# Kernel tuning notes

Hardware: AMD Instinct MI355X
Metric: run time of the kernel (lower is better)

Reference implementation:

```python
import jax, jax.numpy as jnp
import numpy as np


def fps(x, k):
    """Farthest point sampling. x: [B, N, D]. Returns int32 indices [B, k].
    Deterministic: first selected point is index 0 (torch repo uses randint init;
    we fix 0 for a reproducible baseline)."""
    B, N, D = x.shape
    binds = jnp.arange(B)

    def step(carry, _):
        dist, far = carry                      # dist: [B, N], far: [B]
        centroid = x[binds, far]               # [B, D]
        d = jnp.sum((x - centroid[:, None, :]) ** 2, axis=-1)  # [B, N]
        dist = jnp.minimum(dist, d)
        nxt = jnp.argmax(dist, axis=-1)
        return (dist, nxt), far

    init = (jnp.full((B, N), jnp.inf, dtype=x.dtype),
            jnp.zeros((B,), dtype=jnp.int32))
    _, idxs = jax.lax.scan(step, init, None, length=k)
    return idxs.T                              # [B, k]


def sine_mlp(x, params, w0=1.0):
    """Stack of 1x1 convs (== per-point linear) with sin(w0*.) activations.
    x: [B, N, C_in] -> [B, N, C_out]."""
    h = x
    for W, b in params:                        # W: [C_out, C_in], b: [C_out]
        h = jnp.sin(w0 * (jnp.einsum('bnc,oc->bno', h, W) + b))
    return h


_DIMS = [(6, 32), (32, 64), (64, 64), (64, 128), (128, 256), (256, 512)]


def setup_inputs() -> dict:
    key = jax.random.key(0)
    keys = jax.random.split(key, 1 + 2 * len(_DIMS))
    inp = {"x": jax.random.normal(keys[0], (16, 8192, 6), dtype=jnp.float32)}
    for i, (cin, cout) in enumerate(_DIMS):
        scale = 1.0 / np.sqrt(cin)
        inp[f"W{i+1}"] = jax.random.normal(keys[1 + 2 * i], (cout, cin), dtype=jnp.float32) * scale
        inp[f"b{i+1}"] = jax.random.normal(keys[2 + 2 * i], (cout,), dtype=jnp.float32) * 0.01
    inp["k"] = 1024
    return inp


def reference(x, W1, b1, W2, b2, W3, b3, W4, b4, W5, b5, W6, b6, k):
    params = [(W1, b1), (W2, b2), (W3, b3), (W4, b4), (W5, b5), (W6, b6)]
    sample_idx = fps(x, k)                     # [B, k] int32
    feat = sine_mlp(x, params)                 # [B, N, 512]
    # index_points gather along point dim, then permute back -> [B, k, 512]
    out = jnp.take_along_axis(feat, sample_idx[:, :, None], axis=1)
    return out
```

## Files before the change

### kernel.cpp

```cpp
#include <hip/hip_runtime.h>
#include <hip/hip_bf16.h>

#define NPTS 8192
#define KS   1024
#define NB   16
#define MLPB 2048

template<int NT, int JP, int CINP, int CINT, int COUT, int CT, bool LAST>
__device__ __forceinline__ void run_layer(const float* __restrict__ W,
                                          const float* __restrict__ bias,
                                          const float* __restrict__ in,
                                          float* __restrict__ outlds,
                                          float* __restrict__ gout,
                                          float* __restrict__ wt,
                                          int qbase, int tid) {
  constexpr int S = (COUT + 63) / 64;
  const int lane = tid & 63;
  const int wave = tid >> 6;
  const int p0   = wave * JP;

  float acc[JP][S];
  {
    float bv[S];
    #pragma unroll
    for (int s = 0; s < S; ++s) {
      int o = s * 64 + lane;
      bv[s] = (o < COUT) ? bias[o] : 0.f;
    }
    #pragma unroll
    for (int j = 0; j < JP; ++j)
      #pragma unroll
      for (int s = 0; s < S; ++s) acc[j][s] = bv[s];
  }

  for (int ct0 = 0; ct0 < CINT; ct0 += CT) {
    __syncthreads();
    #pragma unroll 1
    for (int e = tid; e < COUT * CT; e += NT) {
      int o  = e / CT;
      int cc = e % CT;
      wt[cc * (COUT + 1) + o] = W[o * CINT + ct0 + cc];
    }
    __syncthreads();
    #pragma unroll
    for (int cc0 = 0; cc0 < CT; cc0 += 4) {
      if (CT - cc0 >= 4) {
        float a[JP][4];
        #pragma unroll
        for (int j = 0; j < JP; ++j) {
          float4 t = *reinterpret_cast<const float4*>(&in[(p0 + j) * CINP + ct0 + cc0]);
          a[j][0] = t.x; a[j][1] = t.y; a[j][2] = t.z; a[j][3] = t.w;
        }
        #pragma unroll
        for (int u = 0; u < 4; ++u) {
          float wvv[S];
          #pragma unroll
          for (int s = 0; s < S; ++s)
            wvv[s] = wt[(cc0 + u) * (COUT + 1) + s * 64 + lane];
          #pragma unroll
          for (int j = 0; j < JP; ++j)
            #pragma unroll
            for (int s = 0; s < S; ++s)
              acc[j][s] = fmaf(a[j][u], wvv[s], acc[j][s]);
        }
      } else {
        float a[JP][2];
        #pragma unroll
        for (int j = 0; j < JP; ++j) {
          float2 t = *reinterpret_cast<const float2*>(&in[(p0 + j) * CINP + ct0 + cc0]);
          a[j][0] = t.x; a[j][1] = t.y;
        }
        #pragma unroll
        for (int u = 0; u < 2; ++u) {
          float wvv[S];
          #pragma unroll
          for (int s = 0; s < S; ++s)
            wvv[s] = wt[(cc0 + u) * (COUT + 1) + s * 64 + lane];
          #pragma unroll
          for (int j = 0; j < JP; ++j)
            #pragma unroll
            for (int s = 0; s < S; ++s)
              acc[j][s] = fmaf(a[j][u], wvv[s], acc[j][s]);
        }
      }
    }
  }
  #pragma unroll
  for (int j = 0; j < JP; ++j) {
    #pragma unroll
    for (int s = 0; s < S; ++s) {
      int o = s * 64 + lane;
      if (o < COUT) {
        float r = sinf(acc[j][s]);
        if (LAST) gout[(size_t)(qbase + p0 + j) * 512 + o] = r;
        else      outlds[(p0 + j) * COUT + o] = r;
      }
    }
  }
}

__device__ __forceinline__ void fps_body(const float* __restrict__ x,
                                         int* __restrict__ idx_out,
                                         unsigned long long* __restrict__ wvi,
                                         int b, int tid) {
#pragma clang fp contract(off)
  const int lane = tid & 63;
  const int wave = tid >> 6;
  const float* xb = x + (size_t)b * NPTS * 6;

  float crd[48];
  {
    const float4* src = reinterpret_cast<const float4*>(xb + tid * 48);
    #pragma unroll
    for (int i = 0; i < 12; ++i) {
      float4 v = src[i];
      crd[4*i+0] = v.x; crd[4*i+1] = v.y; crd[4*i+2] = v.z; crd[4*i+3] = v.w;
    }
  }
  #pragma unroll
  for (int i = 0; i < 48; ++i) asm volatile("" : "+v"(crd[i]));

  float dist[8];
  #pragma unroll
  for (int j = 0; j < 8; ++j) dist[j] = __builtin_huge_valf();

  if (tid == 0) idx_out[b * KS] = 0;
  int bi = 0;

  for (int step = 0; step < KS - 1; ++step) {
    const float* cp = xb + bi * 6;
    const float c0 = cp[0], c1 = cp[1], c2 = cp[2],
                c3 = cp[3], c4 = cp[4], c5 = cp[5];

    float bestv = -1.0f;
    int   besti = 0;
    #pragma unroll
    for (int j = 0; j < 8; ++j) {
      float t0 = crd[6*j+0] - c0; float s = t0 * t0;
      float t1 = crd[6*j+1] - c1; s = s + t1 * t1;
      float t2 = crd[6*j+2] - c2; s = s + t2 * t2;
      float t3 = crd[6*j+3] - c3; s = s + t3 * t3;
      float t4 = crd[6*j+4] - c4; s = s + t4 * t4;
      float t5 = crd[6*j+5] - c5; s = s + t5 * t5;
      float nd = fminf(dist[j], s);
      dist[j] = nd;
      if (nd > bestv) { bestv = nd; besti = tid * 8 + j; }
    }

    unsigned long long pk =
        ((unsigned long long)__float_as_uint(bestv) << 32) | (unsigned)(~besti);
    #pragma unroll
    for (int off = 1; off < 64; off <<= 1) {
      unsigned long long o = __shfl_xor(pk, off, 64);
      if (o > pk) pk = o;
    }
    if (lane == 0) wvi[(step & 1) * 16 + wave] = pk;
    __syncthreads();

    unsigned long long cr = (lane < 16) ? wvi[(step & 1) * 16 + lane] : 0ull;
    #pragma unroll
    for (int off = 1; off < 16; off <<= 1) {
      unsigned long long o = __shfl_xor(cr, off, 64);
      if (o > cr) cr = o;
    }
    bi = ~__builtin_amdgcn_readfirstlane((unsigned)cr);
    if (tid == 0) idx_out[b * KS + step + 1] = bi;
  }
}

__global__ __launch_bounds__(1024, 1) void fused_kernel(
    const float* __restrict__ x, int* __restrict__ idx_out,
    float* __restrict__ feat,
    const float* __restrict__ W1, const float* __restrict__ B1,
    const float* __restrict__ W2, const float* __restrict__ B2,
    const float* __restrict__ W3, const float* __restrict__ B3,
    const float* __restrict__ W4, const float* __restrict__ B4,
    const float* __restrict__ W5, const float* __restrict__ B5,
    const float* __restrict__ W6, const float* __restrict__ B6) {
  __shared__ __align__(16) float A[64 * 128];
  __shared__ float Bb[64 * 256];
  __shared__ float wt[16 * 513];
  const int tid = threadIdx.x;

  if (blockIdx.x < NB) {
    fps_body(x, idx_out, reinterpret_cast<unsigned long long*>(A), blockIdx.x, tid);
    return;
  }

  const int qbase = (blockIdx.x - NB) * 64;
  if (tid < 64) {
    const float* xr = x + (size_t)(qbase + tid) * 6;
    #pragma unroll
    for (int d = 0; d < 6; ++d) A[tid * 8 + d] = xr[d];
  }
  run_layer<1024, 4, 8,   6,  32,  6, false>(W1, B1, A,  Bb, nullptr, wt, qbase, tid);
  run_layer<1024, 4, 32,  32,  64, 16, false>(W2, B2, Bb, A,  nullptr, wt, qbase, tid);
  run_layer<1024, 4, 64,  64,  64, 16, false>(W3, B3, A,  Bb, nullptr, wt, qbase, tid);
  run_layer<1024, 4, 64,  64, 128, 16, false>(W4, B4, Bb, A,  nullptr, wt, qbase, tid);
  run_layer<1024, 4, 128, 128, 256, 16, false>(W5, B5, A,  Bb, nullptr, wt, qbase, tid);
  run_layer<1024, 4, 256, 256, 512, 16, true >(W6, B6, Bb, nullptr, feat, wt, qbase, tid);
}

__global__ __launch_bounds__(256) void gather_kernel(const float* __restrict__ feat,
                                                     const int* __restrict__ sidx,
                                                     float* __restrict__ out) {
  const int r = blockIdx.x * 2 + (threadIdx.x >> 7);
  const int c = (threadIdx.x & 127) * 4;
  const int b = r >> 10;
  const int id = sidx[r];
  const float4 v = *reinterpret_cast<const float4*>(feat + ((size_t)(b * NPTS + id)) * 512 + c);
  *reinterpret_cast<float4*>(out + (size_t)r * 512 + c) = v;
}

__global__ __launch_bounds__(1024, 1) void fps_kernel(const float* __restrict__ x,
                                                      int* __restrict__ idx_out) {
  __shared__ unsigned long long wvi[2 * 16];
  fps_body(x, idx_out, wvi, blockIdx.x, threadIdx.x);
}

__global__ __launch_bounds__(512, 1) void mlp_kernel(
    const float* __restrict__ x, const int* __restrict__ sidx,
    const float* __restrict__ W1, const float* __restrict__ B1,
    const float* __restrict__ W2, const float* __restrict__ B2,
    const float* __restrict__ W3, const float* __restrict__ B3,
    const float* __restrict__ W4, const float* __restrict__ B4,
    const float* __restrict__ W5, const float* __restrict__ B5,
    const float* __restrict__ W6, const float* __restrict__ B6,
    float* __restrict__ out) {
  __shared__ float A[64 * 128];
  __shared__ float Bb[64 * 256];
  __shared__ float wt[16 * 513];
  const int tid   = threadIdx.x;
  const int qbase = blockIdx.x * 64;

  if (tid < 64) {
    int q  = qbase + tid;
    int bb = q >> 10;
    int id = sidx[q];
    const float* xr = x + ((size_t)bb * NPTS + id) * 6;
    #pragma unroll
    for (int d = 0; d < 6; ++d) A[tid * 8 + d] = xr[d];
  }
  run_layer<512, 8, 8,   6,  32,  6, false>(W1, B1, A,  Bb, nullptr, wt, qbase, tid);
  run_layer<512, 8, 32,  32,  64, 16, false>(W2, B2, Bb, A,  nullptr, wt, qbase, tid);
  run_layer<512, 8, 64,  64,  64, 16, false>(W3, B3, A,  Bb, nullptr, wt, qbase, tid);
  run_layer<512, 8, 64,  64, 128, 16, false>(W4, B4, Bb, A,  nullptr, wt, qbase, tid);
  run_layer<512, 8, 128, 128, 256, 16, false>(W5, B5, A,  Bb, nullptr, wt, qbase, tid);
  run_layer<512, 8, 256, 256, 512, 16, true >(W6, B6, Bb, nullptr, out, wt, qbase, tid);
}

extern "C" void kernel_launch(void* const* d_in, const int* in_sizes, int n_in,
                              void* d_out, int out_size, void* d_ws, size_t ws_size,
                              hipStream_t stream) {
  const float* x  = (const float*)d_in[0];
  const float* W1 = (const float*)d_in[1];  const float* B1 = (const float*)d_in[2];
  const float* W2 = (const float*)d_in[3];  const float* B2 = (const float*)d_in[4];
  const float* W3 = (const float*)d_in[5];  const float* B3 = (const float*)d_in[6];
  const float* W4 = (const float*)d_in[7];  const float* B4 = (const float*)d_in[8];
  const float* W5 = (const float*)d_in[9];  const float* B5 = (const float*)d_in[10];
  const float* W6 = (const float*)d_in[11]; const float* B6 = (const float*)d_in[12];
  int*   idxbuf = (int*)d_ws;
  float* out    = (float*)d_out;

  const size_t featBytes = (size_t)NB * NPTS * 512 * sizeof(float);
  if (ws_size >= 65536 + featBytes) {
    float* feat = (float*)((char*)d_ws + 65536);
    fused_kernel<<<NB + MLPB, 1024, 0, stream>>>(x, idxbuf, feat,
                                                 W1, B1, W2, B2, W3, B3,
                                                 W4, B4, W5, B5, W6, B6);
    gather_kernel<<<8192, 256, 0, stream>>>(feat, idxbuf, out);
  } else {
    fps_kernel<<<NB, 1024, 0, stream>>>(x, idxbuf);
    mlp_kernel<<<256, 512, 0, stream>>>(x, idxbuf,
                                        W1, B1, W2, B2, W3, B3,
                                        W4, B4, W5, B5, W6, B6, out);
  }
}
```

Baseline: 2.078 ms.

## Drop fused full-MLP path; run FPS then MLP on sampled points only

```diff
diff --git a/kernel.cpp b/kernel.cpp
--- a/kernel.cpp
+++ b/kernel.cpp
@@ -4,7 +4,81 @@
 #define NPTS 8192
 #define KS   1024
 #define NB   16
-#define MLPB 2048
+
+__global__ __launch_bounds__(1024, 4)
+__attribute__((amdgpu_waves_per_eu(4, 4)))
+void fps_kernel(const float* __restrict__ x, int* __restrict__ idx_out) {
+#pragma clang fp contract(off)
+  const int b    = blockIdx.x;
+  const int tid  = threadIdx.x;
+  const int lane = tid & 63;
+  const int wave = tid >> 6;
+  const float* xb = x + (size_t)b * NPTS * 6;
+
+  float crd[48];
+  {
+    const float4* src = reinterpret_cast<const float4*>(xb + tid * 48);
+    #pragma unroll
+    for (int i = 0; i < 12; ++i) {
+      float4 v = src[i];
+      crd[4*i+0] = v.x; crd[4*i+1] = v.y; crd[4*i+2] = v.z; crd[4*i+3] = v.w;
+    }
+  }
+  #pragma unroll
+  for (int i = 0; i < 48; ++i) asm volatile("" : "+v"(crd[i]));
+
+  float dist[8];
+  #pragma unroll
+  for (int j = 0; j < 8; ++j) dist[j] = __builtin_huge_valf();
+
+  __shared__ uint2 wvi[2][16];
+
+  if (tid == 0) idx_out[b * KS] = 0;
+  int bi = 0;
+
+  for (int step = 0; step < KS - 1; ++step) {
+    const float* cp = xb + bi * 6;
+    const float c0 = cp[0], c1 = cp[1], c2 = cp[2],
+                c3 = cp[3], c4 = cp[4], c5 = cp[5];
+
+    float bestv = -1.0f;
+    int   besti = 0;
+    #pragma unroll
+    for (int j = 0; j < 8; ++j) {
+      float t0 = crd[6*j+0] - c0; float s = t0 * t0;
+      float t1 = crd[6*j+1] - c1; s = s + t1 * t1;
+      float t2 = crd[6*j+2] - c2; s = s + t2 * t2;
+      float t3 = crd[6*j+3] - c3; s = s + t3 * t3;
+      float t4 = crd[6*j+4] - c4; s = s + t4 * t4;
+      float t5 = crd[6*j+5] - c5; s = s + t5 * t5;
+      float nd = fminf(dist[j], s);
+      dist[j] = nd;
+      if (nd > bestv) { bestv = nd; besti = tid * 8 + j; }
+    }
+
+    float wmax = bestv;
+    #pragma unroll
+    for (int off = 1; off < 64; off <<= 1)
+      wmax = fmaxf(wmax, __shfl_xor(wmax, off, 64));
+    unsigned long long ball = __ballot(bestv == wmax);
+    int wlane = (int)__builtin_ctzll(ball);
+    int widx  = __builtin_amdgcn_readlane(besti, wlane);
+
+    if (lane == 0) wvi[step & 1][wave] = make_uint2((unsigned)widx, __float_as_uint(wmax));
+    __syncthreads();
+
+    uint2 wr = wvi[step & 1][lane & 15];
+    float cv = __uint_as_float(wr.y);
+    #pragma unroll
+    for (int off = 1; off < 16; off <<= 1)
+      cv = fmaxf(cv, __shfl_xor(cv, off, 64));
+    unsigned long long b2 = __ballot(__uint_as_float(wr.y) == cv);
+    int cl = (int)__builtin_ctzll(b2);
+    bi = __builtin_amdgcn_readlane((int)wr.x, cl);
+
+    if (tid == 0) idx_out[b * KS + step + 1] = bi;
+  }
+}
 
 template<int NT, int JP, int CINP, int CINT, int COUT, int CT, bool LAST>
 __device__ __forceinline__ void run_layer(const float* __restrict__ W,
@@ -97,125 +171,6 @@
       }
     }
   }
-}
-
-__device__ __forceinline__ void fps_body(const float* __restrict__ x,
-                                         int* __restrict__ idx_out,
-                                         unsigned long long* __restrict__ wvi,
-                                         int b, int tid) {
-#pragma clang fp contract(off)
-  const int lane = tid & 63;
-  const int wave = tid >> 6;
-  const float* xb = x + (size_t)b * NPTS * 6;
-
-  float crd[48];
-  {
-    const float4* src = reinterpret_cast<const float4*>(xb + tid * 48);
-    #pragma unroll
-    for (int i = 0; i < 12; ++i) {
-      float4 v = src[i];
-      crd[4*i+0] = v.x; crd[4*i+1] = v.y; crd[4*i+2] = v.z; crd[4*i+3] = v.w;
-    }
-  }
-  #pragma unroll
-  for (int i = 0; i < 48; ++i) asm volatile("" : "+v"(crd[i]));
-
-  float dist[8];
-  #pragma unroll
-  for (int j = 0; j < 8; ++j) dist[j] = __builtin_huge_valf();
-
-  if (tid == 0) idx_out[b * KS] = 0;
-  int bi = 0;
-
-  for (int step = 0; step < KS - 1; ++step) {
-    const float* cp = xb + bi * 6;
-    const float c0 = cp[0], c1 = cp[1], c2 = cp[2],
-                c3 = cp[3], c4 = cp[4], c5 = cp[5];
-
-    float bestv = -1.0f;
-    int   besti = 0;
-    #pragma unroll
-    for (int j = 0; j < 8; ++j) {
-      float t0 = crd[6*j+0] - c0; float s = t0 * t0;
-      float t1 = crd[6*j+1] - c1; s = s + t1 * t1;
-      float t2 = crd[6*j+2] - c2; s = s + t2 * t2;
-      float t3 = crd[6*j+3] - c3; s = s + t3 * t3;
-      float t4 = crd[6*j+4] - c4; s = s + t4 * t4;
-      float t5 = crd[6*j+5] - c5; s = s + t5 * t5;
-      float nd = fminf(dist[j], s);
-      dist[j] = nd;
-      if (nd > bestv) { bestv = nd; besti = tid * 8 + j; }
-    }
-
-    unsigned long long pk =
-        ((unsigned long long)__float_as_uint(bestv) << 32) | (unsigned)(~besti);
-    #pragma unroll
-    for (int off = 1; off < 64; off <<= 1) {
-      unsigned long long o = __shfl_xor(pk, off, 64);
-      if (o > pk) pk = o;
-    }
-    if (lane == 0) wvi[(step & 1) * 16 + wave] = pk;
-    __syncthreads();
-
-    unsigned long long cr = (lane < 16) ? wvi[(step & 1) * 16 + lane] : 0ull;
-    #pragma unroll
-    for (int off = 1; off < 16; off <<= 1) {
-      unsigned long long o = __shfl_xor(cr, off, 64);
-      if (o > cr) cr = o;
-    }
-    bi = ~__builtin_amdgcn_readfirstlane((unsigned)cr);
-    if (tid == 0) idx_out[b * KS + step + 1] = bi;
-  }
-}
-
-__global__ __launch_bounds__(1024, 1) void fused_kernel(
-    const float* __restrict__ x, int* __restrict__ idx_out,
-    float* __restrict__ feat,
-    const float* __restrict__ W1, const float* __restrict__ B1,
-    const float* __restrict__ W2, const float* __restrict__ B2,
-    const float* __restrict__ W3, const float* __restrict__ B3,
-    const float* __restrict__ W4, const float* __restrict__ B4,
-    const float* __restrict__ W5, const float* __restrict__ B5,
-    const float* __restrict__ W6, const float* __restrict__ B6) {
-  __shared__ __align__(16) float A[64 * 128];
-  __shared__ float Bb[64 * 256];
-  __shared__ float wt[16 * 513];
-  const int tid = threadIdx.x;
-
-  if (blockIdx.x < NB) {
-    fps_body(x, idx_out, reinterpret_cast<unsigned long long*>(A), blockIdx.x, tid);
-    return;
-  }
-
-  const int qbase = (blockIdx.x - NB) * 64;
-  if (tid < 64) {
-    const float* xr = x + (size_t)(qbase + tid) * 6;
-    #pragma unroll
-    for (int d = 0; d < 6; ++d) A[tid * 8 + d] = xr[d];
-  }
-  run_layer<1024, 4, 8,   6,  32,  6, false>(W1, B1, A,  Bb, nullptr, wt, qbase, tid);
-  run_layer<1024, 4, 32,  32,  64, 16, false>(W2, B2, Bb, A,  nullptr, wt, qbase, tid);
-  run_layer<1024, 4, 64,  64,  64, 16, false>(W3, B3, A,  Bb, nullptr, wt, qbase, tid);
-  run_layer<1024, 4, 64,  64, 128, 16, false>(W4, B4, Bb, A,  nullptr, wt, qbase, tid);
-  run_layer<1024, 4, 128, 128, 256, 16, false>(W5, B5, A,  Bb, nullptr, wt, qbase, tid);
-  run_layer<1024, 4, 256, 256, 512, 16, true >(W6, B6, Bb, nullptr, feat, wt, qbase, tid);
-}
-
-__global__ __launch_bounds__(256) void gather_kernel(const float* __restrict__ feat,
-                                                     const int* __restrict__ sidx,
-                                                     float* __restrict__ out) {
-  const int r = blockIdx.x * 2 + (threadIdx.x >> 7);
-  const int c = (threadIdx.x & 127) * 4;
-  const int b = r >> 10;
-  const int id = sidx[r];
-  const float4 v = *reinterpret_cast<const float4*>(feat + ((size_t)(b * NPTS + id)) * 512 + c);
-  *reinterpret_cast<float4*>(out + (size_t)r * 512 + c) = v;
-}
-
-__global__ __launch_bounds__(1024, 1) void fps_kernel(const float* __restrict__ x,
-                                                      int* __restrict__ idx_out) {
-  __shared__ unsigned long long wvi[2 * 16];
-  fps_body(x, idx_out, wvi, blockIdx.x, threadIdx.x);
 }
 
 __global__ __launch_bounds__(512, 1) void mlp_kernel(
@@ -262,17 +217,8 @@
   int*   idxbuf = (int*)d_ws;
   float* out    = (float*)d_out;
 
-  const size_t featBytes = (size_t)NB * NPTS * 512 * sizeof(float);
-  if (ws_size >= 65536 + featBytes) {
-    float* feat = (float*)((char*)d_ws + 65536);
-    fused_kernel<<<NB + MLPB, 1024, 0, stream>>>(x, idxbuf, feat,
-                                                 W1, B1, W2, B2, W3, B3,
-                                                 W4, B4, W5, B5, W6, B6);
-    gather_kernel<<<8192, 256, 0, stream>>>(feat, idxbuf, out);
-  } else {
-    fps_kernel<<<NB, 1024, 0, stream>>>(x, idxbuf);
-    mlp_kernel<<<256, 512, 0, stream>>>(x, idxbuf,
-                                        W1, B1, W2, B2, W3, B3,
-                                        W4, B4, W5, B5, W6, B6, out);
-  }
-}
+  fps_kernel<<<NB, 1024, 0, stream>>>(x, idxbuf);
+  mlp_kernel<<<256, 512, 0, stream>>>(x, idxbuf,
+                                      W1, B1, W2, B2, W3, B3,
+                                      W4, B4, W5, B5, W6, B6, out);
+}
```

Result: faster. 1.952 ms (-6.1%).
